# Kernel tuning notes

Measured on AMD Instinct MI355X. Metric: run time of the kernel, lower is better.

The kernel has to match this reference:

```python
import jax, jax.numpy as jnp
import numpy as np

B, H, D, S = 128, 64, 96, 256  # batch, heads, head_dim, num cache slots


def setup_inputs() -> dict:
    key = jax.random.key(0)
    k0, k1, k2, k3, k4, k5 = jax.random.split(key, 6)
    return {
        "q": jax.random.normal(k0, (B, H, 1, D), dtype=jnp.float32),
        "k": jax.random.normal(k1, (B, H, 1, D), dtype=jnp.float32),
        "v": jax.random.normal(k2, (B, H, 1, D), dtype=jnp.float32),
        "kv_caches": jax.random.normal(k3, (S, H, D, D), dtype=jnp.float32),
        "slope_rate": jax.random.uniform(k4, (H,), dtype=jnp.float32),
        "slot_idx": jax.random.randint(k5, (B,), 0, S, dtype=jnp.int32),
    }


def reference(q, k, v, kv_caches, slope_rate, slot_idx):
    # q/k/v: [B,H,1,D] -> [B,H,D]
    q3, k3, v3 = q[:, :, 0], k[:, :, 0], v[:, :, 0]
    valid = slot_idx >= 0                                   # [B]
    safe_slot = jnp.where(valid, slot_idx, 0)
    ratio = jnp.exp(-slope_rate)                            # [H] decay per head
    kv_old = kv_caches[safe_slot]                           # gather: [B,H,D,D]
    # decayed outer-product state update: kv_new = k v^T + exp(-slope)*kv_old
    kv_new = k3[..., :, None] * v3[..., None, :] + ratio[None, :, None, None] * kv_old
    # fused reduce: out[b,h,e] = sum_d q[b,h,d] * kv_new[b,h,d,e]
    out = jnp.einsum('bhd,bhde->bhe', q3, kv_new)
    out = jnp.where(valid[:, None, None], out, 0.0)         # slot_id == -1 -> zeros
    return out[:, :, None, :]                               # [B,H,1,D]
```

## Files before the change

kernel.cpp:

```cpp
#include <hip/hip_runtime.h>


#define NB 128
#define NH 64
#define ND 96
#define NS 256

__global__ __launch_bounds__(128, 4) void la_decode(
    const float* __restrict__ q, const float* __restrict__ k,
    const float* __restrict__ v, const float* __restrict__ kvc,
    const float* __restrict__ slope, const int* __restrict__ slot_idx,
    float* __restrict__ out)
{
    const int bid = blockIdx.x;
    const int h = bid >> 7;
    const int b = bid & (NB - 1);
    const int t = threadIdx.x;

    __shared__ float qs[ND];
    __shared__ float red[128];
    __shared__ float part[4][ND];

    const int slot = slot_idx[b];
    const bool valid = slot >= 0;
    const int safe = valid ? slot : 0;

    const int bh = b * NH + h;

    float p = 0.f;
    if (t < ND) {
        float qv = q[bh * ND + t];
        qs[t] = qv;
        p = qv * k[bh * ND + t];
    }
    red[t] = p;
    __syncthreads();

    #pragma unroll
    for (int s = 64; s > 0; s >>= 1) {
        if (t < s) red[t] += red[t + s];
        __syncthreads();
    }
    const float qk = red[0];

    float4 acc = make_float4(0.f, 0.f, 0.f, 0.f);
    if (t < 96) {
        const int dp = t / 24;
        const int e4 = t % 24;
        const float* __restrict__ kp =
            kvc + ((size_t)safe * NH + h) * (size_t)(ND * ND);
        const float4* __restrict__ kp4 = (const float4*)(kp + 4 * t);
        #pragma unroll 8
        for (int j = 0; j < 24; ++j) {
            const float4 kv4 = kp4[j * 96];
            const float qd = qs[j * 4 + dp];
            acc.x = fmaf(qd, kv4.x, acc.x);
            acc.y = fmaf(qd, kv4.y, acc.y);
            acc.z = fmaf(qd, kv4.z, acc.z);
            acc.w = fmaf(qd, kv4.w, acc.w);
        }
        *(float4*)&part[dp][e4 * 4] = acc;
    }
    __syncthreads();

    if (t < ND) {
        const float dot = part[0][t] + part[1][t] + part[2][t] + part[3][t];
        const float ratio = __expf(-slope[h]);
        const float o = valid ? fmaf(qk, v[bh * ND + t], ratio * dot) : 0.f;
        out[bh * ND + t] = o;
    }
}

extern "C" void kernel_launch(void* const* d_in, const int* in_sizes, int n_in,
                              void* d_out, int out_size, void* d_ws, size_t ws_size,
                              hipStream_t stream) {
    const float* q     = (const float*)d_in[0];
    const float* k     = (const float*)d_in[1];
    const float* v     = (const float*)d_in[2];
    const float* kvc   = (const float*)d_in[3];
    const float* slope = (const float*)d_in[4];
    const int*   slot  = (const int*)d_in[5];
    float* out = (float*)d_out;

    dim3 grid(NB * NH);
    dim3 block(128);
    la_decode<<<grid, block, 0, stream>>>(q, k, v, kvc, slope, slot, out);
}
```

Baseline: 701.3 us.

## Bin batches by cache slot so each KV tile is read once per slot

Adds a single-block pre-pass that groups batch indices by slot into a workspace histogram and lists. The main kernel then runs one block per (slot, head) and reuses each loaded KV tile for up to four batches per chunk, writing zeros for invalid slots. This cuts duplicate KV-cache reads when several batches share a slot. In exchange it adds an extra launch, serial small reductions, and many idle blocks for empty slots.

```diff
diff --git a/kernel.cpp b/kernel.cpp
--- a/kernel.cpp
+++ b/kernel.cpp
@@ -5,69 +5,127 @@
 #define NH 64
 #define ND 96
 #define NS 256
+#define CH 4
+
+
+__global__ __launch_bounds__(256) void bin_slots(const int* __restrict__ slot_idx,
+                                                 int* __restrict__ cnt,
+                                                 int* __restrict__ lists) {
+    __shared__ int lc[NS + 1];
+    const int t = threadIdx.x;
+    for (int i = t; i < NS + 1; i += 256) lc[i] = 0;
+    __syncthreads();
+    if (t < NB) {
+        const int s = slot_idx[t];
+        const int idx = (s >= 0 && s < NS) ? s : NS;
+        const int p = atomicAdd(&lc[idx], 1);
+        lists[idx * NB + p] = t;
+    }
+    __syncthreads();
+    for (int i = t; i < NS + 1; i += 256) cnt[i] = lc[i];
+}
 
 __global__ __launch_bounds__(128, 4) void la_decode(
     const float* __restrict__ q, const float* __restrict__ k,
     const float* __restrict__ v, const float* __restrict__ kvc,
-    const float* __restrict__ slope, const int* __restrict__ slot_idx,
-    float* __restrict__ out)
+    const float* __restrict__ slope, const int* __restrict__ cnt,
+    const int* __restrict__ lists, float* __restrict__ out)
 {
-    const int bid = blockIdx.x;
-    const int h = bid >> 7;
-    const int b = bid & (NB - 1);
+    const int s = blockIdx.x;
+    const int h = blockIdx.y;
     const int t = threadIdx.x;
 
-    __shared__ float qs[ND];
-    __shared__ float red[128];
-    __shared__ float part[4][ND];
+    const int c = cnt[s];
+    if (c == 0) return;
 
-    const int slot = slot_idx[b];
-    const bool valid = slot >= 0;
-    const int safe = valid ? slot : 0;
+    if (s == NS) {
+        for (int i = 0; i < c; ++i) {
+            const int b = lists[NS * NB + i];
+            if (t < ND) out[((size_t)b * NH + h) * ND + t] = 0.f;
+        }
+        return;
+    }
 
-    const int bh = b * NH + h;
+    __shared__ float qt[ND][CH];
+    __shared__ float ks[CH][100];
+    __shared__ float qk[CH];
+    __shared__ float part[4][CH][ND];
 
-    float p = 0.f;
-    if (t < ND) {
-        float qv = q[bh * ND + t];
-        qs[t] = qv;
-        p = qv * k[bh * ND + t];
-    }
-    red[t] = p;
-    __syncthreads();
+    const float ratio = __expf(-slope[h]);
+    const float* __restrict__ tile = kvc + ((size_t)s * NH + h) * (size_t)(ND * ND);
 
-    #pragma unroll
-    for (int s = 64; s > 0; s >>= 1) {
-        if (t < s) red[t] += red[t + s];
+    const int dp = t / 24;
+    const int e4 = t % 24;
+
+    for (int cb = 0; cb < c; cb += CH) {
+        const int cc = min(CH, c - cb);
         __syncthreads();
-    }
-    const float qk = red[0];
 
-    float4 acc = make_float4(0.f, 0.f, 0.f, 0.f);
-    if (t < 96) {
-        const int dp = t / 24;
-        const int e4 = t % 24;
-        const float* __restrict__ kp =
-            kvc + ((size_t)safe * NH + h) * (size_t)(ND * ND);
-        const float4* __restrict__ kp4 = (const float4*)(kp + 4 * t);
-        #pragma unroll 8
-        for (int j = 0; j < 24; ++j) {
-            const float4 kv4 = kp4[j * 96];
-            const float qd = qs[j * 4 + dp];
-            acc.x = fmaf(qd, kv4.x, acc.x);
-            acc.y = fmaf(qd, kv4.y, acc.y);
-            acc.z = fmaf(qd, kv4.z, acc.z);
-            acc.w = fmaf(qd, kv4.w, acc.w);
+        if (t < ND) {
+            #pragma unroll
+            for (int bi = 0; bi < CH; ++bi) {
+                if (bi < cc) {
+                    const int b = lists[s * NB + cb + bi];
+                    const size_t off = ((size_t)b * NH + h) * ND + t;
+                    qt[t][bi] = q[off];
+                    ks[bi][t] = k[off];
+                } else {
+                    qt[t][bi] = 0.f;
+                    ks[bi][t] = 0.f;
+                }
+            }
         }
-        *(float4*)&part[dp][e4 * 4] = acc;
-    }
-    __syncthreads();
+        __syncthreads();
 
-    if (t < ND) {
-        const float dot = part[0][t] + part[1][t] + part[2][t] + part[3][t];
-        const float ratio = __expf(-slope[h]);
-        const float o = valid ? fmaf(qk, v[bh * ND + t], ratio * dot) : 0.f;
-        out[bh * ND + t] = o;
+        if (t < CH) {
+            float d = 0.f;
+            for (int i = 0; i < ND; ++i) d += qt[i][t] * ks[t][i];
+            qk[t] = d;
+        }
+        __syncthreads();
+
+        float4 acc[CH];
+        #pragma unroll
+        for (int bi = 0; bi < CH; ++bi) acc[bi] = make_float4(0.f, 0.f, 0.f, 0.f);
+
+        if (t < 96) {
+            const float4* __restrict__ tp4 = (const float4*)(tile + 4 * t);
+            #pragma unroll 8
+            for (int j = 0; j < 24; ++j) {
+                const float4 kv4 = tp4[j * 96];
+                const float4 qd = *(const float4*)&qt[4 * j + dp][0];
+                acc[0].x = fmaf(qd.x, kv4.x, acc[0].x);
+                acc[0].y = fmaf(qd.x, kv4.y, acc[0].y);
+                acc[0].z = fmaf(qd.x, kv4.z, acc[0].z);
+                acc[0].w = fmaf(qd.x, kv4.w, acc[0].w);
+                acc[1].x = fmaf(qd.y, kv4.x, acc[1].x);
+                acc[1].y = fmaf(qd.y, kv4.y, acc[1].y);
+                acc[1].z = fmaf(qd.y, kv4.z, acc[1].z);
+                acc[1].w = fmaf(qd.y, kv4.w, acc[1].w);
+                acc[2].x = fmaf(qd.z, kv4.x, acc[2].x);
+                acc[2].y = fmaf(qd.z, kv4.y, acc[2].y);
+                acc[2].z = fmaf(qd.z, kv4.z, acc[2].z);
+                acc[2].w = fmaf(qd.z, kv4.w, acc[2].w);
+                acc[3].x = fmaf(qd.w, kv4.x, acc[3].x);
+                acc[3].y = fmaf(qd.w, kv4.y, acc[3].y);
+                acc[3].z = fmaf(qd.w, kv4.z, acc[3].z);
+                acc[3].w = fmaf(qd.w, kv4.w, acc[3].w);
+            }
+            #pragma unroll
+            for (int bi = 0; bi < CH; ++bi)
+                *(float4*)&part[dp][bi][e4 * 4] = acc[bi];
+        }
+        __syncthreads();
+
+        if (t < ND) {
+            for (int bi = 0; bi < cc; ++bi) {
+                const int b = lists[s * NB + cb + bi];
+                const float dot = part[0][bi][t] + part[1][bi][t]
+                                + part[2][bi][t] + part[3][bi][t];
+                const size_t off = ((size_t)b * NH + h) * ND + t;
+                out[off] = fmaf(qk[bi], v[off], ratio * dot);
+            }
+        }
     }
 }
 
@@ -82,7 +140,11 @@
     const int*   slot  = (const int*)d_in[5];
     float* out = (float*)d_out;
 
-    dim3 grid(NB * NH);
-    dim3 block(128);
-    la_decode<<<grid, block, 0, stream>>>(q, k, v, kvc, slope, slot, out);
+    int* cnt   = (int*)d_ws;
+    int* lists = cnt + (NS + 1);
+
+    bin_slots<<<1, 256, 0, stream>>>(slot, cnt, lists);
+
+    dim3 grid(NS + 1, NH);
+    la_decode<<<grid, dim3(128), 0, stream>>>(q, k, v, kvc, slope, cnt, lists, out);
 }
```

Measured after the change: 703.3 us. About the same (+0.3%).
